# Optimization experiments

Hardware: AMD Instinct MI355X
Metric: run time of the kernel (lower is better)

Reference implementation:

```python
import jax, jax.numpy as jnp
import numpy as np

B, L, D = 2, 2048, 2048
H, KV = 32, 8
HD = D // H          # 64
REP = H // KV        # 4


def setup_inputs() -> dict:
    key = jax.random.key(0)
    ks = jax.random.split(key, 6)
    x = jax.random.normal(ks[0], (B, L, D), dtype=jnp.float32)
    # weights stored [in, out] (transpose of torch Linear weight), scaled for stability
    wq = jax.random.normal(ks[1], (D, H * HD), dtype=jnp.float32) * 0.02
    wk = jax.random.normal(ks[2], (D, KV * HD), dtype=jnp.float32) * 0.02
    wv = jax.random.normal(ks[3], (D, KV * HD), dtype=jnp.float32) * 0.02
    wo = jax.random.normal(ks[4], (H * HD, D), dtype=jnp.float32) * 0.02
    # RoPE frequencies: freqs_cis = exp(i * pos * theta), theta_j = 10000^{-2j/HD}
    inv_freq = 1.0 / (10000.0 ** (jnp.arange(0, HD, 2, dtype=jnp.float32) / HD))  # [HD/2]
    angles = jnp.arange(L, dtype=jnp.float32)[:, None] * inv_freq[None, :]        # [L, HD/2]
    freqs_cos = jnp.cos(angles)
    freqs_sin = jnp.sin(angles)
    # additive causal mask [L, L] (prefill from start_pos=0)
    mask = jnp.where(jnp.tril(jnp.ones((L, L), dtype=bool)), 0.0, -jnp.inf).astype(jnp.float32)
    return {"x": x, "start_pos": 0, "freqs_cos": freqs_cos, "freqs_sin": freqs_sin,
            "mask": mask, "wq": wq, "wk": wk, "wv": wv, "wo": wo}


def _apply_rope(t, cos, sin):
    # t: [B, L, h, HD]; cos/sin: [L, HD/2] -> broadcast [1, L, 1, HD/2]
    tp = t.reshape(*t.shape[:-1], HD // 2, 2)
    a, b = tp[..., 0], tp[..., 1]
    c = cos[None, :, None, :]
    s = sin[None, :, None, :]
    ra = a * c - b * s
    rb = a * s + b * c
    return jnp.stack([ra, rb], axis=-1).reshape(t.shape)


def reference(x, start_pos, freqs_cos, freqs_sin, mask, wq, wk, wv, wo):
    xq = jnp.einsum('bld,de->ble', x, wq).reshape(B, L, H, HD)
    xk = jnp.einsum('bld,de->ble', x, wk).reshape(B, L, KV, HD)
    xv = jnp.einsum('bld,de->ble', x, wv).reshape(B, L, KV, HD)
    xq = _apply_rope(xq, freqs_cos, freqs_sin)
    xk = _apply_rope(xk, freqs_cos, freqs_sin)
    # (cache write of xk/xv is a dead side effect in the torch module; omitted)
    # GQA: query head (g*REP + r) attends to kv head g  == repeat_interleave semantics
    q = xq.transpose(0, 2, 1, 3).reshape(B, KV, REP, L, HD)  # [B,KV,REP,L,HD]
    k = xk.transpose(0, 2, 1, 3)                              # [B,KV,L,HD]
    v = xv.transpose(0, 2, 1, 3)
    scale = 1.0 / jnp.sqrt(jnp.float32(HD))
    scores = jnp.einsum('bgrld,bgmd->bgrlm', q, k) * scale + mask  # [B,KV,REP,L,L]
    attn = jax.nn.softmax(scores, axis=-1)
    out = jnp.einsum('bgrlm,bgmd->bgrld', attn, v)            # [B,KV,REP,L,HD]
    out = out.reshape(B, H, L, HD).transpose(0, 2, 1, 3).reshape(B, L, H * HD)
    return jnp.einsum('ble,ed->bld', out, wo)
```

## Files before the change

kernel.cpp:

```cpp
#include <hip/hip_runtime.h>
#include <hip/hip_bf16.h>
#include <math.h>

typedef __bf16 bf16_t;
typedef __bf16 bf16x8 __attribute__((ext_vector_type(8)));
typedef __bf16 bf16x4 __attribute__((ext_vector_type(4)));
typedef __bf16 bf16x2 __attribute__((ext_vector_type(2)));
typedef float  f32x4  __attribute__((ext_vector_type(4)));
typedef int    i32x4  __attribute__((ext_vector_type(4)));

#define B_  2
#define L_  2048
#define D_  2048
#define H_  32
#define KV_ 8
#define HD_ 64

static __device__ __forceinline__ void gload_lds16(const bf16_t* g, void* l)
{
    __builtin_amdgcn_global_load_lds(
        (const __attribute__((address_space(1))) void*)g,
        (__attribute__((address_space(3))) void*)l, 16, 0, 0);
}

static __device__ __forceinline__ int packbf(float a, float b)
{
    bf16x2 t; t[0] = (bf16_t)a; t[1] = (bf16_t)b;
    return __builtin_bit_cast(int, t);
}

__global__ void cast_f32_bf16(const float4* __restrict__ in,
                              bf16x4* __restrict__ out, int n4)
{
    const int i = blockIdx.x * 256 + threadIdx.x;
    if (i >= n4) return;
    const float4 v = in[i];
    bf16x4 o;
    o[0] = (bf16_t)v.x; o[1] = (bf16_t)v.y; o[2] = (bf16_t)v.z; o[3] = (bf16_t)v.w;
    out[i] = o;
}

template <typename InT>
__global__ void transpose_cast(const InT* __restrict__ in, bf16_t* __restrict__ out,
                               int R, int C)
{
    __shared__ bf16_t tile[32][33];
    const int bx = blockIdx.x * 32, by = blockIdx.y * 32;
    in  += (size_t)blockIdx.z * R * C;
    out += (size_t)blockIdx.z * R * C;
    const int tx = threadIdx.x, ty = threadIdx.y;
#pragma unroll
    for (int i = ty; i < 32; i += 8)
        tile[i][tx] = (bf16_t)(float)in[(size_t)(by + i) * C + bx + tx];
    __syncthreads();
#pragma unroll
    for (int i = ty; i < 32; i += 8)
        out[(size_t)(bx + i) * R + by + tx] = tile[tx][i];
}

template <typename OutT>
__global__ __launch_bounds__(256) void gemm_tn(
    const bf16_t* __restrict__ A,
    const bf16_t* __restrict__ BT,
    OutT* __restrict__ C,
    int M, int N, int K)
{
    __shared__ __attribute__((aligned(16))) bf16_t As[128 * 32];
    __shared__ __attribute__((aligned(16))) bf16_t Bs[128 * 32];

    const int m0   = blockIdx.y * 128;
    const int n0   = blockIdx.x * 128;
    const int tid  = threadIdx.x;
    const int wave = tid >> 6;
    const int lane = tid & 63;
    const int quad = lane >> 4;
    const int l16  = lane & 15;
    const int wm   = (wave & 1) * 64;
    const int wn   = (wave >> 1) * 64;
    const int sr   = tid >> 2;
    const int sc   = (tid & 3) * 8;

    f32x4 acc[4][4];
    const f32x4 zf = {0.f, 0.f, 0.f, 0.f};
#pragma unroll
    for (int i = 0; i < 4; i++)
#pragma unroll
        for (int j = 0; j < 4; j++) acc[i][j] = zf;

    const bf16_t* ag = A  + (size_t)(m0 + sr) * K + sc;
    const bf16_t* bg = BT + (size_t)(n0 + sr) * K + sc;
    bf16_t* asl = As + tid * 8;
    bf16_t* bsl = Bs + tid * 8;

    for (int k0 = 0; k0 < K; k0 += 32) {
        gload_lds16(ag + k0,                  asl);
        gload_lds16(ag + (size_t)64 * K + k0, asl + 2048);
        gload_lds16(bg + k0,                  bsl);
        gload_lds16(bg + (size_t)64 * K + k0, bsl + 2048);
        __syncthreads();

        bf16x8 af[4], bfr[4];
#pragma unroll
        for (int i = 0; i < 4; i++)
            af[i] = *(const bf16x8*)(&As[(wm + i * 16 + l16) * 32 + quad * 8]);
#pragma unroll
        for (int i = 0; i < 4; i++)
            bfr[i] = *(const bf16x8*)(&Bs[(wn + i * 16 + l16) * 32 + quad * 8]);

#pragma unroll
        for (int mi = 0; mi < 4; mi++)
#pragma unroll
            for (int ni = 0; ni < 4; ni++)
                acc[mi][ni] = __builtin_amdgcn_mfma_f32_16x16x32_bf16(
                    af[mi], bfr[ni], acc[mi][ni], 0, 0, 0);
        __syncthreads();
    }

#pragma unroll
    for (int mi = 0; mi < 4; mi++)
#pragma unroll
        for (int ni = 0; ni < 4; ni++)
#pragma unroll
            for (int r = 0; r < 4; r++) {
                const int row = m0 + wm + mi * 16 + quad * 4 + r;
                const int col = n0 + wn + ni * 16 + l16;
                C[(size_t)row * N + col] = (OutT)acc[mi][ni][r];
            }
}

__global__ __launch_bounds__(256) void gemm_qkv(
    const bf16_t* __restrict__ A,
    const bf16_t* __restrict__ BT,
    bf16_t* __restrict__ Qb, bf16_t* __restrict__ Kb, bf16_t* __restrict__ Vb,
    int K)
{
    __shared__ __attribute__((aligned(16))) bf16_t As[128 * 32];
    __shared__ __attribute__((aligned(16))) bf16_t Bs[128 * 32];

    const int m0   = blockIdx.y * 128;
    const int n0   = blockIdx.x * 128;
    const int tid  = threadIdx.x;
    const int wave = tid >> 6;
    const int lane = tid & 63;
    const int quad = lane >> 4;
    const int l16  = lane & 15;
    const int wm   = (wave & 1) * 64;
    const int wn   = (wave >> 1) * 64;
    const int sr   = tid >> 2;
    const int sc   = (tid & 3) * 8;

    f32x4 acc[4][4];
    const f32x4 zf = {0.f, 0.f, 0.f, 0.f};
#pragma unroll
    for (int i = 0; i < 4; i++)
#pragma unroll
        for (int j = 0; j < 4; j++) acc[i][j] = zf;

    const bf16_t* ag = A  + (size_t)(m0 + sr) * K + sc;
    const bf16_t* bg = BT + (size_t)(n0 + sr) * K + sc;
    bf16_t* asl = As + tid * 8;
    bf16_t* bsl = Bs + tid * 8;

    for (int k0 = 0; k0 < K; k0 += 32) {
        gload_lds16(ag + k0,                  asl);
        gload_lds16(ag + (size_t)64 * K + k0, asl + 2048);
        gload_lds16(bg + k0,                  bsl);
        gload_lds16(bg + (size_t)64 * K + k0, bsl + 2048);
        __syncthreads();

        bf16x8 af[4], bfr[4];
#pragma unroll
        for (int i = 0; i < 4; i++)
            af[i] = *(const bf16x8*)(&As[(wm + i * 16 + l16) * 32 + quad * 8]);
#pragma unroll
        for (int i = 0; i < 4; i++)
            bfr[i] = *(const bf16x8*)(&Bs[(wn + i * 16 + l16) * 32 + quad * 8]);

#pragma unroll
        for (int mi = 0; mi < 4; mi++)
#pragma unroll
            for (int ni = 0; ni < 4; ni++)
                acc[mi][ni] = __builtin_amdgcn_mfma_f32_16x16x32_bf16(
                    af[mi], bfr[ni], acc[mi][ni], 0, 0, 0);
        __syncthreads();
    }

    bf16_t* Cb; int ldc, coff;
    if (n0 < 2048)      { Cb = Qb; ldc = 2048; coff = 0; }
    else if (n0 < 2560) { Cb = Kb; ldc = 512;  coff = 2048; }
    else                { Cb = Vb; ldc = 512;  coff = 2560; }

#pragma unroll
    for (int mi = 0; mi < 4; mi++)
#pragma unroll
        for (int ni = 0; ni < 4; ni++)
#pragma unroll
            for (int r = 0; r < 4; r++) {
                const int row = m0 + wm + mi * 16 + quad * 4 + r;
                const int col = n0 + wn + ni * 16 + l16 - coff;
                Cb[(size_t)row * ldc + col] = (bf16_t)acc[mi][ni][r];
            }
}

__global__ void rope_k(bf16_t* __restrict__ T, const float* __restrict__ fc,
                       const float* __restrict__ fs, int nheads, int total8)
{
    const int idx = blockIdx.x * 256 + threadIdx.x;
    if (idx >= total8) return;
    const int g  = idx & 7;
    const int t  = idx >> 3;
    const int h  = t % nheads;
    const int bl = t / nheads;
    const int l  = bl & (L_ - 1);
    const float4 c4 = *(const float4*)(fc + l * 32 + g * 4);
    const float4 s4 = *(const float4*)(fs + l * 32 + g * 4);
    const size_t off = ((size_t)bl * nheads + h) * 64 + g * 8;
    const bf16x8 v = *(const bf16x8*)(T + off);
    const float cc[4] = {c4.x, c4.y, c4.z, c4.w};
    const float ss[4] = {s4.x, s4.y, s4.z, s4.w};
    bf16x8 o;
#pragma unroll
    for (int p = 0; p < 4; p++) {
        const float a  = (float)v[2 * p];
        const float b2 = (float)v[2 * p + 1];
        o[2 * p]     = (bf16_t)(a * cc[p] - b2 * ss[p]);
        o[2 * p + 1] = (bf16_t)(a * ss[p] + b2 * cc[p]);
    }
    *(bf16x8*)(T + off) = o;
}

__global__ __launch_bounds__(256, 2) void attn_k(
    const bf16_t* __restrict__ Q,
    const bf16_t* __restrict__ Kc,
    const bf16_t* __restrict__ VT,
    bf16_t* __restrict__ Ob)
{
    __shared__ __attribute__((aligned(16))) char LDS[65536];
    float* OL = (float*)LDS;
    float* LR = (float*)(LDS + 17408);

    const int tid  = threadIdx.x;
    const int wave = tid >> 6;
    const int lane = tid & 63;
    const int quad = lane >> 4;
    const int l16  = lane & 15;
    const int c    = blockIdx.x;
    const int bh   = blockIdx.y;
    const int bb   = bh >> 5;
    const int h    = bh & 31;
    const int kvh  = h >> 2;
    const size_t bbL = (size_t)bb * L_;

    const int scol = (((tid & 3) ^ ((tid >> 3) & 3)) * 8);
    const int sw16 = ((l16 >> 1) & 3) * 16;

    const bf16_t* Kg  = Kc + (bbL + (tid >> 2)) * (KV_ * HD_) + kvh * HD_ + scol;
    const bf16_t* Vg  = VT + (size_t)(bb * KV_ + kvh) * HD_ * L_ + (size_t)(tid >> 2) * L_ + scol;
    const f32x4 zf = {0.f, 0.f, 0.f, 0.f};

    for (int half = 0; half < 2; ++half) {
        const int j     = half ? c : 31 - c;
        const int qbase = j * 64;
        const int nkt   = (j + 2) >> 1;

        bf16x8 qf[4][2];
#pragma unroll
        for (int qt = 0; qt < 4; qt++) {
            const bf16_t* qrow = Q + ((bbL + qbase + qt * 16 + l16) * H_ + h) * HD_;
#pragma unroll
            for (int cc = 0; cc < 2; cc++) {
                bf16x8 v = *(const bf16x8*)(qrow + cc * 32 + quad * 8);
#pragma unroll
                for (int i = 0; i < 8; i++) v[i] = (bf16_t)((float)v[i] * 0.125f);
                qf[qt][cc] = v;
            }
        }

        f32x4 acc[4][4];
#pragma unroll
        for (int mt = 0; mt < 4; mt++)
#pragma unroll
            for (int qt = 0; qt < 4; qt++) acc[mt][qt] = zf;
        float lacc[4] = {0.f, 0.f, 0.f, 0.f};

        {
            char* kb = LDS;
#pragma unroll
            for (int cc = 0; cc < 2; cc++)
#pragma unroll
                for (int hh = 0; hh < 2; hh++)
                    gload_lds16(Kg + (size_t)(hh * 64) * (KV_ * HD_) + cc * 32,
                                kb + cc * 8192 + hh * 4096 + tid * 16);
#pragma unroll
            for (int kc = 0; kc < 4; kc++)
                gload_lds16(Vg + kc * 32, kb + 16384 + kc * 4096 + tid * 16);
        }

        for (int kt = 0; kt < nkt; kt++) {
            __syncthreads();

            if (kt + 1 < nkt) {
                char* kb = LDS + ((kt + 1) & 1) * 32768;
                const size_t ko = (size_t)(kt + 1) * 128;
#pragma unroll
                for (int cc = 0; cc < 2; cc++)
#pragma unroll
                    for (int hh = 0; hh < 2; hh++)
                        gload_lds16(Kg + (ko + hh * 64) * (KV_ * HD_) + cc * 32,
                                    kb + cc * 8192 + hh * 4096 + tid * 16);
#pragma unroll
                for (int kc = 0; kc < 4; kc++)
                    gload_lds16(Vg + ko + kc * 32, kb + 16384 + kc * 4096 + tid * 16);
            }

            const char* Kld = LDS + (kt & 1) * 32768;
            const char* Vld = Kld + 16384;

            bf16x8 kf[2][2];
#pragma unroll
            for (int t = 0; t < 2; t++)
#pragma unroll
                for (int cc = 0; cc < 2; cc++)
                    kf[t][cc] = *(const bf16x8*)(Kld + cc * 8192 +
                        (wave * 32 + t * 16 + l16) * 64 + ((quad * 16) ^ sw16));

            f32x4 st[2][4];
            __builtin_amdgcn_s_setprio(1);
#pragma unroll
            for (int t = 0; t < 2; t++)
#pragma unroll
                for (int qt = 0; qt < 4; qt++) {
                    f32x4 s = __builtin_amdgcn_mfma_f32_16x16x32_bf16(
                        kf[t][0], qf[qt][0], zf, 0, 0, 0);
                    st[t][qt] = __builtin_amdgcn_mfma_f32_16x16x32_bf16(
                        kf[t][1], qf[qt][1], s, 0, 0, 0);
                }
            __builtin_amdgcn_s_setprio(0);

            bf16x8 vf[4];
#pragma unroll
            for (int mt = 0; mt < 4; mt++)
                vf[mt] = *(const bf16x8*)(Vld + wave * 4096 +
                    (mt * 16 + l16) * 64 + ((quad * 16) ^ sw16));

            if (kt == nkt - 1) {
                const int kq = kt * 128 + wave * 32 + quad * 4 - qbase - l16;
#pragma unroll
                for (int t = 0; t < 2; t++)
#pragma unroll
                    for (int qt = 0; qt < 4; qt++)
#pragma unroll
                        for (int r = 0; r < 4; r++)
                            st[t][qt][r] = (kq + t * 16 - qt * 16 + r <= 0)
                                         ? st[t][qt][r] : -__builtin_inff();
            }

            int pk[2][4][2];
#pragma unroll
            for (int t = 0; t < 2; t++)
#pragma unroll
                for (int qt = 0; qt < 4; qt++) {
                    const float e0 = __expf(st[t][qt][0]);
                    const float e1 = __expf(st[t][qt][1]);
                    const float e2 = __expf(st[t][qt][2]);
                    const float e3 = __expf(st[t][qt][3]);
                    lacc[qt] += (e0 + e1) + (e2 + e3);
                    pk[t][qt][0] = packbf(e0, e1);
                    pk[t][qt][1] = packbf(e2, e3);
                }

            const int s1 = ((quad & 1) * 2) * 16 + l16;
            const int s2 = s1 + 16;
            const bool hi = quad >= 2;
#pragma unroll
            for (int qt = 0; qt < 4; qt++) {
                const int a0 = __shfl(pk[0][qt][0], s1);
                const int a1 = __shfl(pk[0][qt][1], s1);
                const int b0 = __shfl(pk[1][qt][0], s1);
                const int b1 = __shfl(pk[1][qt][1], s1);
                const int c0 = __shfl(pk[0][qt][0], s2);
                const int c1 = __shfl(pk[0][qt][1], s2);
                const int d0 = __shfl(pk[1][qt][0], s2);
                const int d1 = __shfl(pk[1][qt][1], s2);
                i32x4 bi;
                bi[0] = hi ? b0 : a0;
                bi[1] = hi ? b1 : a1;
                bi[2] = hi ? d0 : c0;
                bi[3] = hi ? d1 : c1;
                const bf16x8 pb = __builtin_bit_cast(bf16x8, bi);
                __builtin_amdgcn_s_setprio(1);
#pragma unroll
                for (int mt = 0; mt < 4; mt++)
                    acc[mt][qt] = __builtin_amdgcn_mfma_f32_16x16x32_bf16(
                        vf[mt], pb, acc[mt][qt], 0, 0, 0);
                __builtin_amdgcn_s_setprio(0);
            }
        }

        float lw[4];
#pragma unroll
        for (int qt = 0; qt < 4; qt++) {
            float v = lacc[qt];
            v += __shfl_xor(v, 16);
            v += __shfl_xor(v, 32);
            lw[qt] = v;
        }

        __syncthreads();

        if (quad == 0)
#pragma unroll
            for (int qt = 0; qt < 4; qt++)
                LR[(wave * 4 + qt) * 16 + l16] = lw[qt];

#pragma unroll
        for (int p = 0; p < 4; p++) {
#pragma unroll
            for (int qt = 0; qt < 4; qt++) {
                if (((qt - wave) & 3) == p) {
#pragma unroll
                    for (int mt = 0; mt < 4; mt++) {
                        float* a = OL + (qt * 16 + l16) * 68 + mt * 16 + quad * 4;
                        if (p == 0) *(f32x4*)a = acc[mt][qt];
                        else        *(f32x4*)a = *(f32x4*)a + acc[mt][qt];
                    }
                }
            }
            __syncthreads();
        }

        const float ls = LR[(0 * 4 + wave) * 16 + l16] + LR[(1 * 4 + wave) * 16 + l16]
                       + LR[(2 * 4 + wave) * 16 + l16] + LR[(3 * 4 + wave) * 16 + l16];
        const float inv = 1.f / ls;
        bf16_t* orow = Ob + ((bbL + qbase + wave * 16 + l16) * H_ + h) * HD_;
#pragma unroll
        for (int j2 = 0; j2 < 4; j2++) {
            const f32x4 v = *(const f32x4*)(OL + (wave * 16 + l16) * 68 + quad * 16 + j2 * 4);
            bf16x4 o;
#pragma unroll
            for (int i = 0; i < 4; i++) o[i] = (bf16_t)(v[i] * inv);
            *(bf16x4*)(orow + quad * 16 + j2 * 4) = o;
        }
        __syncthreads();
    }
}

extern "C" void kernel_launch(void* const* d_in, const int* in_sizes, int n_in,
                              void* d_out, int out_size, void* d_ws, size_t ws_size,
                              hipStream_t stream)
{
    (void)in_sizes; (void)n_in; (void)out_size; (void)ws_size;
    const float* xf = (const float*)d_in[0];
    const float* fc = (const float*)d_in[2];
    const float* fs = (const float*)d_in[3];
    const float* wq = (const float*)d_in[5];
    const float* wk = (const float*)d_in[6];
    const float* wv = (const float*)d_in[7];
    const float* wo = (const float*)d_in[8];
    float* out = (float*)d_out;

    char* ws = (char*)d_ws;
    bf16_t* xb   = (bf16_t*)(ws);
    bf16_t* Qb   = (bf16_t*)(ws + (16ull << 20));
    bf16_t* Kb   = (bf16_t*)(ws + (32ull << 20));
    bf16_t* Vb   = (bf16_t*)(ws + (36ull << 20));
    bf16_t* VTb  = (bf16_t*)(ws + (40ull << 20));
    bf16_t* Oa   = (bf16_t*)(ws + (44ull << 20));
    bf16_t* Wqkv = (bf16_t*)(ws + (60ull << 20));
    bf16_t* WoT  = (bf16_t*)(ws + (72ull << 20));

    cast_f32_bf16<<<8192, 256, 0, stream>>>((const float4*)xf, (bf16x4*)xb,
                                            B_ * L_ * D_ / 4);

    const dim3 tb(32, 8);
    transpose_cast<float><<<dim3(64, 64, 1), tb, 0, stream>>>(wq, Wqkv, 2048, 2048);
    transpose_cast<float><<<dim3(16, 64, 1), tb, 0, stream>>>(wk, Wqkv + 2048ull * 2048, 2048, 512);
    transpose_cast<float><<<dim3(16, 64, 1), tb, 0, stream>>>(wv, Wqkv + 2560ull * 2048, 2048, 512);
    transpose_cast<float><<<dim3(64, 64, 1), tb, 0, stream>>>(wo, WoT, 2048, 2048);

    gemm_qkv<<<dim3(24, 32), 256, 0, stream>>>(xb, Wqkv, Qb, Kb, Vb, 2048);

    rope_k<<<4096, 256, 0, stream>>>(Qb, fc, fs, 32, B_ * L_ * 32 * 8);
    rope_k<<<1024, 256, 0, stream>>>(Kb, fc, fs, 8, B_ * L_ * 8 * 8);

    transpose_cast<bf16_t><<<dim3(16, 64, 2), tb, 0, stream>>>(Vb, VTb, 2048, 512);

    attn_k<<<dim3(16, 64), 256, 0, stream>>>(Qb, Kb, VTb, Oa);

    gemm_tn<float><<<dim3(16, 32), 256, 0, stream>>>(Oa, WoT, out, 4096, 2048, 2048);
}
```

Measured before the change: 367.3 us.

## Load attention K/V directly from global, fold scale into K, use permlane swaps

The attention kernel drops its double-buffered LDS staging of K and V tiles and instead has each wave load its K and V fragments straight from global memory into registers. This shrinks LDS to the epilogue buffer, so occupancy is raised to 3 blocks per SIMD, and block ids are remapped so blocks sharing a KV head run together for cache reuse. The softmax scale and log2(e) are folded into K in the projection epilogue, which allows exp2 and removes the per-element Q scaling. The shuffle-based P repacking is replaced with v_permlane32/16_swap instructions. The cost is more global and L2 traffic with uncoalesced, unswizzled per-wave loads, and a different bf16 rounding point for the scale.

```diff
diff --git a/kernel.cpp b/kernel.cpp
--- a/kernel.cpp
+++ b/kernel.cpp
@@ -27,6 +27,15 @@
 {
     bf16x2 t; t[0] = (bf16_t)a; t[1] = (bf16_t)b;
     return __builtin_bit_cast(int, t);
+}
+
+static __device__ __forceinline__ void pl32(int& a, int& b)
+{
+    asm("v_permlane32_swap_b32 %0, %1" : "+v"(a), "+v"(b));
+}
+static __device__ __forceinline__ void pl16(int& a, int& b)
+{
+    asm("v_permlane16_swap_b32 %0, %1" : "+v"(a), "+v"(b));
 }
 
 __global__ void cast_f32_bf16(const float4* __restrict__ in,
@@ -185,9 +194,10 @@
         __syncthreads();
     }
 
-    bf16_t* Cb; int ldc, coff;
+    bf16_t* Cb; int ldc, coff; float cscale = 1.f;
     if (n0 < 2048)      { Cb = Qb; ldc = 2048; coff = 0; }
-    else if (n0 < 2560) { Cb = Kb; ldc = 512;  coff = 2048; }
+    else if (n0 < 2560) { Cb = Kb; ldc = 512;  coff = 2048;
+                          cscale = 0.18033688011112042f; }
     else                { Cb = Vb; ldc = 512;  coff = 2560; }
 
 #pragma unroll
@@ -198,7 +208,7 @@
             for (int r = 0; r < 4; r++) {
                 const int row = m0 + wm + mi * 16 + quad * 4 + r;
                 const int col = n0 + wn + ni * 16 + l16 - coff;
-                Cb[(size_t)row * ldc + col] = (bf16_t)acc[mi][ni][r];
+                Cb[(size_t)row * ldc + col] = (bf16_t)(acc[mi][ni][r] * cscale);
             }
 }
 
@@ -229,13 +239,13 @@
     *(bf16x8*)(T + off) = o;
 }
 
-__global__ __launch_bounds__(256, 2) void attn_k(
+__global__ __launch_bounds__(256, 3) void attn_k(
     const bf16_t* __restrict__ Q,
     const bf16_t* __restrict__ Kc,
     const bf16_t* __restrict__ VT,
     bf16_t* __restrict__ Ob)
 {
-    __shared__ __attribute__((aligned(16))) char LDS[65536];
+    __shared__ __attribute__((aligned(16))) char LDS[18432];
     float* OL = (float*)LDS;
     float* LR = (float*)(LDS + 17408);
 
@@ -244,18 +254,17 @@
     const int lane = tid & 63;
     const int quad = lane >> 4;
     const int l16  = lane & 15;
-    const int c    = blockIdx.x;
-    const int bh   = blockIdx.y;
+
+    const int id   = blockIdx.y * 16 + blockIdx.x;
+    const int c    = (id >> 3) & 15;
+    const int bh   = (id & 7) * 8 + (id >> 7);
     const int bb   = bh >> 5;
     const int h    = bh & 31;
     const int kvh  = h >> 2;
     const size_t bbL = (size_t)bb * L_;
 
-    const int scol = (((tid & 3) ^ ((tid >> 3) & 3)) * 8);
-    const int sw16 = ((l16 >> 1) & 3) * 16;
-
-    const bf16_t* Kg  = Kc + (bbL + (tid >> 2)) * (KV_ * HD_) + kvh * HD_ + scol;
-    const bf16_t* Vg  = VT + (size_t)(bb * KV_ + kvh) * HD_ * L_ + (size_t)(tid >> 2) * L_ + scol;
+    const bf16_t* Kg = Kc + bbL * (KV_ * HD_) + kvh * HD_;
+    const bf16_t* Vg = VT + (size_t)(bb * KV_ + kvh) * HD_ * L_;
     const f32x4 zf = {0.f, 0.f, 0.f, 0.f};
 
     for (int half = 0; half < 2; ++half) {
@@ -267,13 +276,8 @@
 #pragma unroll
         for (int qt = 0; qt < 4; qt++) {
             const bf16_t* qrow = Q + ((bbL + qbase + qt * 16 + l16) * H_ + h) * HD_;
-#pragma unroll
-            for (int cc = 0; cc < 2; cc++) {
-                bf16x8 v = *(const bf16x8*)(qrow + cc * 32 + quad * 8);
-#pragma unroll
-                for (int i = 0; i < 8; i++) v[i] = (bf16_t)((float)v[i] * 0.125f);
-                qf[qt][cc] = v;
-            }
+            qf[qt][0] = *(const bf16x8*)(qrow + quad * 8);
+            qf[qt][1] = *(const bf16x8*)(qrow + 32 + quad * 8);
         }
 
         f32x4 acc[4][4];
@@ -283,46 +287,22 @@
             for (int qt = 0; qt < 4; qt++) acc[mt][qt] = zf;
         float lacc[4] = {0.f, 0.f, 0.f, 0.f};
 
-        {
-            char* kb = LDS;
-#pragma unroll
-            for (int cc = 0; cc < 2; cc++)
-#pragma unroll
-                for (int hh = 0; hh < 2; hh++)
-                    gload_lds16(Kg + (size_t)(hh * 64) * (KV_ * HD_) + cc * 32,
-                                kb + cc * 8192 + hh * 4096 + tid * 16);
-#pragma unroll
-            for (int kc = 0; kc < 4; kc++)
-                gload_lds16(Vg + kc * 32, kb + 16384 + kc * 4096 + tid * 16);
-        }
-
         for (int kt = 0; kt < nkt; kt++) {
-            __syncthreads();
-
-            if (kt + 1 < nkt) {
-                char* kb = LDS + ((kt + 1) & 1) * 32768;
-                const size_t ko = (size_t)(kt + 1) * 128;
+            const int k0 = kt * 128 + wave * 32;
+
+            bf16x8 kf[2][2];
+#pragma unroll
+            for (int t = 0; t < 2; t++)
 #pragma unroll
                 for (int cc = 0; cc < 2; cc++)
-#pragma unroll
-                    for (int hh = 0; hh < 2; hh++)
-                        gload_lds16(Kg + (ko + hh * 64) * (KV_ * HD_) + cc * 32,
-                                    kb + cc * 8192 + hh * 4096 + tid * 16);
-#pragma unroll
-                for (int kc = 0; kc < 4; kc++)
-                    gload_lds16(Vg + ko + kc * 32, kb + 16384 + kc * 4096 + tid * 16);
-            }
-
-            const char* Kld = LDS + (kt & 1) * 32768;
-            const char* Vld = Kld + 16384;
-
-            bf16x8 kf[2][2];
-#pragma unroll
-            for (int t = 0; t < 2; t++)
-#pragma unroll
-                for (int cc = 0; cc < 2; cc++)
-                    kf[t][cc] = *(const bf16x8*)(Kld + cc * 8192 +
-                        (wave * 32 + t * 16 + l16) * 64 + ((quad * 16) ^ sw16));
+                    kf[t][cc] = *(const bf16x8*)(Kg +
+                        (size_t)(k0 + t * 16 + l16) * (KV_ * HD_) + cc * 32 + quad * 8);
+
+            bf16x8 vf[4];
+#pragma unroll
+            for (int mt = 0; mt < 4; mt++)
+                vf[mt] = *(const bf16x8*)(Vg +
+                    (size_t)(mt * 16 + l16) * L_ + k0 + quad * 8);
 
             f32x4 st[2][4];
             __builtin_amdgcn_s_setprio(1);
@@ -337,12 +317,6 @@
                 }
             __builtin_amdgcn_s_setprio(0);
 
-            bf16x8 vf[4];
-#pragma unroll
-            for (int mt = 0; mt < 4; mt++)
-                vf[mt] = *(const bf16x8*)(Vld + wave * 4096 +
-                    (mt * 16 + l16) * 64 + ((quad * 16) ^ sw16));
-
             if (kt == nkt - 1) {
                 const int kq = kt * 128 + wave * 32 + quad * 4 - qbase - l16;
 #pragma unroll
@@ -360,33 +334,23 @@
             for (int t = 0; t < 2; t++)
 #pragma unroll
                 for (int qt = 0; qt < 4; qt++) {
-                    const float e0 = __expf(st[t][qt][0]);
-                    const float e1 = __expf(st[t][qt][1]);
-                    const float e2 = __expf(st[t][qt][2]);
-                    const float e3 = __expf(st[t][qt][3]);
+                    const float e0 = __builtin_amdgcn_exp2f(st[t][qt][0]);
+                    const float e1 = __builtin_amdgcn_exp2f(st[t][qt][1]);
+                    const float e2 = __builtin_amdgcn_exp2f(st[t][qt][2]);
+                    const float e3 = __builtin_amdgcn_exp2f(st[t][qt][3]);
                     lacc[qt] += (e0 + e1) + (e2 + e3);
                     pk[t][qt][0] = packbf(e0, e1);
                     pk[t][qt][1] = packbf(e2, e3);
                 }
 
-            const int s1 = ((quad & 1) * 2) * 16 + l16;
-            const int s2 = s1 + 16;
-            const bool hi = quad >= 2;
 #pragma unroll
             for (int qt = 0; qt < 4; qt++) {
-                const int a0 = __shfl(pk[0][qt][0], s1);
-                const int a1 = __shfl(pk[0][qt][1], s1);
-                const int b0 = __shfl(pk[1][qt][0], s1);
-                const int b1 = __shfl(pk[1][qt][1], s1);
-                const int c0 = __shfl(pk[0][qt][0], s2);
-                const int c1 = __shfl(pk[0][qt][1], s2);
-                const int d0 = __shfl(pk[1][qt][0], s2);
-                const int d1 = __shfl(pk[1][qt][1], s2);
+                int a0 = pk[0][qt][0], b0 = pk[1][qt][0];
+                pl32(a0, b0); pl16(a0, b0);
+                int a1 = pk[0][qt][1], b1 = pk[1][qt][1];
+                pl32(a1, b1); pl16(a1, b1);
                 i32x4 bi;
-                bi[0] = hi ? b0 : a0;
-                bi[1] = hi ? b1 : a1;
-                bi[2] = hi ? d0 : c0;
-                bi[3] = hi ? d1 : c1;
+                bi[0] = a0; bi[1] = a1; bi[2] = b0; bi[3] = b1;
                 const bf16x8 pb = __builtin_bit_cast(bf16x8, bi);
                 __builtin_amdgcn_s_setprio(1);
 #pragma unroll
```

Measured after the change: 384.1 us. 1.05x slower.
